# Performance work log

Measured on AMD Instinct MI355X. Metric: run time of the kernel, lower is better.

## Reference

```python
import jax, jax.numpy as jnp
import numpy as np

# static config matching init_kwargs
NODE, K, KER, STR = 32, 10, 5, 2
B, C = 8, 64
N = NODE * NODE          # 1024 nodes per sample
BN = B * N               # 8192 total nodes
OUT = (NODE - KER) // STR + 1
E = OUT * OUT            # local hyperedges per sample (196)
BN_EPS = 1e-5


def _local_block_diag():
    """Static block-diagonal local incidence matrix (BN, B*E), built once in numpy."""
    idx = np.arange(N).reshape(NODE, NODE)
    H_local = np.zeros((N, E), np.float32)
    e = 0
    for i in range(0, NODE - KER + 1, STR):
        for j in range(0, NODE - KER + 1, STR):
            H_local[idx[i:i + KER, j:j + KER].ravel(), e] = 1.0
            e += 1
    blk = np.zeros((BN, B * E), np.float32)
    for b in range(B):
        blk[b * N:(b + 1) * N, b * E:(b + 1) * E] = H_local
    return jnp.asarray(blk)


_LOCAL_BLK = _local_block_diag()


def setup_inputs() -> dict:
    key = jax.random.key(0)
    k1, k2 = jax.random.split(key, 2)
    x = jax.random.normal(k1, (B, N, C), jnp.float32)
    W_conv = jax.random.normal(k2, (C, C), jnp.float32) * 0.05
    b_conv = jnp.zeros((C,), jnp.float32)
    gamma = jnp.ones((C,), jnp.float32)
    beta = jnp.zeros((C,), jnp.float32)
    return {"x": x, "W_conv": W_conv, "b_conv": b_conv, "gamma": gamma, "beta": beta}


def reference(x, W_conv, b_conv, gamma, beta):
    xm = x.reshape(BN, C)                       # merged nodes (B*N, C)

    # --- hypergraph construction (no_grad in torch) ---
    xs = jax.lax.stop_gradient(xm)
    sq = jnp.sum(xs * xs, axis=-1, keepdims=True)
    dists = sq - 2.0 * (xs @ xs.T) + sq.T       # (BN, BN) pairwise sq-dists
    _, inds = jax.lax.top_k(-dists, K + 1)      # K+1 smallest distances
    # weights_function(prob=False) -> all ones; scatter incidence
    H = jnp.zeros((BN, BN), x.dtype).at[jnp.arange(BN)[:, None], inds].set(1.0)
    # Dv == K+1 for every row -> max_k = K+1 and the second topk gives new_H == H
    Hfull = jnp.concatenate([H, _LOCAL_BLK], axis=1)  # (BN, BN + B*E)

    # G = Dv^{-1/2} H W De^{-1} H^T Dv^{-1/2}, W = I, via diagonal scaling
    DV = Hfull.sum(axis=1)
    DE = jnp.maximum(Hfull.sum(axis=0), 1e-8)
    dv2 = DV ** -0.5
    A = dv2[:, None] * Hfull
    G = (A * (1.0 / DE)[None, :]) @ A.T          # (BN, BN)
    G = jax.lax.stop_gradient(G)

    # --- HGNN conv: linear -> G matmul -> BN (train stats) -> relu -> residual ---
    y = xm @ W_conv.T + b_conv                   # (BN, C)
    z = G @ y                                    # (BN, C)
    mu = z.mean(axis=0)
    var = z.var(axis=0)                          # biased, as torch BN training
    zn = (z - mu) / jnp.sqrt(var + BN_EPS) * gamma + beta
    out = jax.nn.relu(zn) + xm
    return out.reshape(B, N, C)
```

## Files before the change

### kernel.cpp

```cpp
#include <hip/hip_runtime.h>
#include <math.h>

#define BNTOT 8192
#define CH    64
#define KP1   11
#define NLOC  1568
#define CAP   1024
#define LCAP  64
#define MARGIN 2.5f

typedef __attribute__((ext_vector_type(8))) short short8;
typedef __attribute__((ext_vector_type(4))) float float4v;

__device__ __forceinline__ int pcnt(int p) {
  int lo = p - 4; if (lo < 0) lo = 0; lo += (lo & 1);
  int hi = p; if (hi > 26) hi = 26;
  return (hi >= lo) ? (((hi - lo) >> 1) + 1) : 0;
}
__device__ __forceinline__ float dv2_of(int u) {
  int node = u & 1023;
  int rr = node >> 5, cc = node & 31;
  int dv = KP1 + pcnt(rr) * pcnt(cc);
  return 1.0f / sqrtf((float)dv);
}
__device__ __forceinline__ unsigned short f2bf(float f) {
  unsigned u = __float_as_uint(f);
  unsigned r = (u + 0x7FFFu + ((u >> 16) & 1u)) >> 16;
  return (unsigned short)r;
}
__device__ __forceinline__ unsigned long long skey(float s, int idx) {
  unsigned u = __float_as_uint(s);
  u = (u & 0x80000000u) ? ~u : (u | 0x80000000u);
  return ((unsigned long long)u << 32) | (unsigned)idx;
}

__global__ void k_cast(const float* __restrict__ X, unsigned short* __restrict__ Xh,
                       float* __restrict__ sq) {
  int g = blockIdx.x * 256 + threadIdx.x;
  int lane = threadIdx.x & 63;
  float v = X[g];
  Xh[g] = f2bf(v);
  float s = v * v;
  #pragma unroll
  for (int off = 32; off >= 1; off >>= 1) s += __shfl_xor(s, off, 64);
  if (lane == 0) sq[g >> 6] = s;
}

__global__ __launch_bounds__(256)
void k_thrpart(const float* __restrict__ X, const float* __restrict__ sq,
               float* __restrict__ part) {
  const int tid = threadIdx.x, wave = tid >> 6, lane = tid & 63;
  const int rg = blockIdx.x >> 3, chunk = blockIdx.x & 7;
  const int row = rg * 64 + lane;
  float xr[CH];
  {
    const float4* xp = (const float4*)(X + (size_t)row * CH);
    #pragma unroll
    for (int k = 0; k < CH / 4; ++k) {
      float4 v = xp[k];
      xr[4*k+0] = v.x; xr[4*k+1] = v.y; xr[4*k+2] = v.z; xr[4*k+3] = v.w;
    }
  }
  float tv[KP1];
  #pragma unroll
  for (int t = 0; t < KP1; ++t) tv[t] = INFINITY;

  for (int s = 0; s < 32; ++s) {
    int j = __builtin_amdgcn_readfirstlane(((chunk * 4 + wave) * 32 + s) * 8);
    const float* cp = X + (size_t)j * CH;
    float d0 = 0.f, d1 = 0.f, d2 = 0.f, d3 = 0.f;
    #pragma unroll
    for (int k = 0; k < CH / 4; ++k) {
      d0 = fmaf(xr[4*k+0], cp[4*k+0], d0);
      d1 = fmaf(xr[4*k+1], cp[4*k+1], d1);
      d2 = fmaf(xr[4*k+2], cp[4*k+2], d2);
      d3 = fmaf(xr[4*k+3], cp[4*k+3], d3);
    }
    float cv = fmaf(-2.0f, (d0 + d1) + (d2 + d3), sq[j]);
    #pragma unroll
    for (int t = 0; t < KP1; ++t) {
      float lo = fminf(tv[t], cv), hi = fmaxf(tv[t], cv);
      tv[t] = lo; cv = hi;
    }
  }
  __shared__ float ls[4][64][KP1];
  #pragma unroll
  for (int t = 0; t < KP1; ++t) ls[wave][lane][t] = tv[t];
  __syncthreads();
  if (tid < 64) {
    float v[KP1];
    #pragma unroll
    for (int t = 0; t < KP1; ++t) v[t] = ls[0][tid][t];
    #pragma unroll
    for (int w = 1; w < 4; ++w)
      #pragma unroll
      for (int t = 0; t < KP1; ++t) {
        float cv = ls[w][tid][t];
        #pragma unroll
        for (int s2 = 0; s2 < KP1; ++s2) {
          float lo = fminf(v[s2], cv), hi = fmaxf(v[s2], cv);
          v[s2] = lo; cv = hi;
        }
      }
    size_t base = ((size_t)blockIdx.x * 64 + tid) * KP1;
    #pragma unroll
    for (int t = 0; t < KP1; ++t) part[base + t] = v[t];
  }
}

__global__ void k_thrmerge(const float* __restrict__ part, float* __restrict__ thr) {
  const int rg = blockIdx.x, lane = threadIdx.x;
  const int row = rg * 64 + lane;
  float v[KP1];
  {
    size_t b0 = ((size_t)(rg * 8) * 64 + lane) * KP1;
    #pragma unroll
    for (int t = 0; t < KP1; ++t) v[t] = part[b0 + t];
  }
  for (int c = 1; c < 8; ++c) {
    size_t b = ((size_t)(rg * 8 + c) * 64 + lane) * KP1;
    #pragma unroll
    for (int t = 0; t < KP1; ++t) {
      float cv = part[b + t];
      #pragma unroll
      for (int s2 = 0; s2 < KP1; ++s2) {
        float lo = fminf(v[s2], cv), hi = fmaxf(v[s2], cv);
        v[s2] = lo; cv = hi;
      }
    }
  }
  thr[row] = v[KP1 - 1] + MARGIN;
}

__global__ __launch_bounds__(256)
void k_filter(const unsigned short* __restrict__ Xh, const float* __restrict__ sq,
              const float* __restrict__ thr, int* __restrict__ cnt,
              unsigned short* __restrict__ cand) {
  __shared__ unsigned short lcand[64][LCAP + 2];
  __shared__ int lcnt[64];
  __shared__ int lbase[64];

  const int tid = threadIdx.x, wave = tid >> 6, lane = tid & 63;
  const int m = lane & 15, q = lane >> 4;
  const int rowbase = (blockIdx.x >> 5) * 64;
  const int colbase = (blockIdx.x & 31) * 256 + wave * 64;

  if (tid < 64) lcnt[tid] = 0;

  short8 a[4][2];
  #pragma unroll
  for (int rt = 0; rt < 4; ++rt)
    #pragma unroll
    for (int kc = 0; kc < 2; ++kc)
      a[rt][kc] = *(const short8*)(Xh + (size_t)(rowbase + rt * 16 + m) * CH + kc * 32 + q * 8);

  short8 b0[4], b1[4];
  float sqv[4];
  #pragma unroll
  for (int sub = 0; sub < 4; ++sub) {
    const int coln = colbase + sub * 16 + m;
    const short8* bp = (const short8*)(Xh + (size_t)coln * CH + q * 8);
    b0[sub] = bp[0];
    b1[sub] = bp[4];
    sqv[sub] = sq[coln];
  }

  float thrv[16];
  #pragma unroll
  for (int rt = 0; rt < 4; ++rt)
    #pragma unroll
    for (int r = 0; r < 4; ++r)
      thrv[rt * 4 + r] = thr[rowbase + rt * 16 + q * 4 + r];

  __syncthreads();

  const float4v cz = {0.f, 0.f, 0.f, 0.f};
  #pragma unroll
  for (int sub = 0; sub < 4; ++sub) {
    const int coln = colbase + sub * 16 + m;
    #pragma unroll
    for (int rt = 0; rt < 4; ++rt) {
      float4v c = __builtin_amdgcn_mfma_f32_16x16x32_bf16(a[rt][0], b0[sub], cz, 0, 0, 0);
      c = __builtin_amdgcn_mfma_f32_16x16x32_bf16(a[rt][1], b1[sub], c, 0, 0, 0);
      #pragma unroll
      for (int r = 0; r < 4; ++r) {
        float score = fmaf(-2.0f, c[r], sqv[sub]);
        if (score < thrv[rt * 4 + r]) {
          int rl = rt * 16 + q * 4 + r;
          int s = atomicAdd(&lcnt[rl], 1);
          if (s < LCAP) {
            lcand[rl][s] = (unsigned short)coln;
          } else {
            int gs = atomicAdd(&cnt[rowbase + rl], 1);
            if (gs < CAP) cand[(size_t)(rowbase + rl) * CAP + gs] = (unsigned short)coln;
          }
        }
      }
    }
  }

  __syncthreads();
  if (tid < 64) {
    int nl = lcnt[tid]; if (nl > LCAP) nl = LCAP;
    lbase[tid] = atomicAdd(&cnt[rowbase + tid], nl);
    lcnt[tid] = nl;
  }
  __syncthreads();
  if (tid < 64) {
    int nl = lcnt[tid], base = lbase[tid];
    unsigned short* dst = cand + (size_t)(rowbase + tid) * CAP;
    for (int s = 0; s < nl; ++s) {
      int g = base + s;
      if (g < CAP) dst[g] = lcand[tid][s];
    }
  }
}

__global__ __launch_bounds__(256)
void k_rescore(const float* __restrict__ X, const float* __restrict__ sq,
               const int* __restrict__ cnt, const unsigned short* __restrict__ cand,
               int* __restrict__ inds, int* __restrict__ DE) {
  const int tid = threadIdx.x, lane = tid & 63;
  const int row = __builtin_amdgcn_readfirstlane(blockIdx.x * 4 + (tid >> 6));

  float xr[CH];
  {
    const float4* xp = (const float4*)(X + (size_t)row * CH);
    #pragma unroll
    for (int k = 0; k < CH / 4; ++k) {
      float4 v = xp[k];
      xr[4*k+0] = v.x; xr[4*k+1] = v.y; xr[4*k+2] = v.z; xr[4*k+3] = v.w;
    }
  }
  int n = cnt[row]; if (n > CAP) n = CAP;

  float tv[KP1]; int ti[KP1];
  #pragma unroll
  for (int t = 0; t < KP1; ++t) { tv[t] = INFINITY; ti[t] = -1; }

  for (int s = lane; s < n; s += 64) {
    int cj = cand[(size_t)row * CAP + s];
    const float4* cp = (const float4*)(X + (size_t)cj * CH);
    float d0 = 0.f, d1 = 0.f, d2 = 0.f, d3 = 0.f;
    #pragma unroll
    for (int k = 0; k < CH / 4; ++k) {
      float4 v = cp[k];
      d0 = fmaf(xr[4*k+0], v.x, d0);
      d1 = fmaf(xr[4*k+1], v.y, d1);
      d2 = fmaf(xr[4*k+2], v.z, d2);
      d3 = fmaf(xr[4*k+3], v.w, d3);
    }
    float score = fmaf(-2.0f, (d0 + d1) + (d2 + d3), sq[cj]);
    if (score < tv[KP1 - 1]) {
      float cv = score; int ci = cj;
      #pragma unroll
      for (int t = 0; t < KP1; ++t) {
        bool sw = cv < tv[t];
        float nv = sw ? cv   : tv[t]; int ni = sw ? ci   : ti[t];
        float ov = sw ? tv[t] : cv;   int oi = sw ? ti[t] : ci;
        tv[t] = nv; ti[t] = ni; cv = ov; ci = oi;
      }
    }
  }

  unsigned long long cur = skey(tv[0], ti[0]);
  unsigned long long keep = 0;
  #pragma unroll
  for (int t = 0; t < KP1; ++t) {
    unsigned long long m = cur;
    #pragma unroll
    for (int off = 1; off < 64; off <<= 1) {
      unsigned lo = __shfl_xor((unsigned)m, off, 64);
      unsigned hi = __shfl_xor((unsigned)(m >> 32), off, 64);
      unsigned long long o = ((unsigned long long)hi << 32) | lo;
      m = (o < m) ? o : m;
    }
    if (lane == t) keep = m;
    if (cur == m) {
      #pragma unroll
      for (int q = 0; q < KP1 - 1; ++q) { tv[q] = tv[q+1]; ti[q] = ti[q+1]; }
      tv[KP1-1] = INFINITY; ti[KP1-1] = -1;
      cur = skey(tv[0], ti[0]);
    }
  }
  if (lane < KP1) {
    int idx = (int)(unsigned)(keep & 0xFFFFFFFFu);
    inds[(size_t)row * KP1 + lane] = idx;
    atomicAdd(&DE[idx], 1);
  }
}

__global__ void k_lin(const float* __restrict__ X, const float* __restrict__ W,
                      const float* __restrict__ bias, float* __restrict__ t) {
  int lane = threadIdx.x & 63;
  int wave = threadIdx.x >> 6;
  int rowbase = (blockIdx.x * 4 + wave) * 16;
  float wr[CH];
  {
    const float4* wp = (const float4*)(W + (size_t)lane * CH);
    #pragma unroll
    for (int k = 0; k < CH / 4; ++k) {
      float4 v = wp[k];
      wr[4*k+0] = v.x; wr[4*k+1] = v.y; wr[4*k+2] = v.z; wr[4*k+3] = v.w;
    }
  }
  float bc = bias[lane];
  for (int r = 0; r < 16; ++r) {
    int row = __builtin_amdgcn_readfirstlane(rowbase + r);
    const float* xp = X + (size_t)row * CH;
    float d0 = 0.f, d1 = 0.f, d2 = 0.f, d3 = 0.f;
    #pragma unroll
    for (int k = 0; k < CH / 4; ++k) {
      d0 = fmaf(wr[4*k+0], xp[4*k+0], d0);
      d1 = fmaf(wr[4*k+1], xp[4*k+1], d1);
      d2 = fmaf(wr[4*k+2], xp[4*k+2], d2);
      d3 = fmaf(wr[4*k+3], xp[4*k+3], d3);
    }
    float y = (d0 + d1) + (d2 + d3) + bc;
    t[(size_t)row * CH + lane] = y * dv2_of(row);
  }
}

__global__ void k_scatter(const float* __restrict__ t, const int* __restrict__ inds,
                          float* __restrict__ s_knn) {
  int c = threadIdx.x & 63;
  int u = blockIdx.x * 4 + (threadIdx.x >> 6);
  float val = t[(size_t)u * CH + c];
  int ub = __builtin_amdgcn_readfirstlane(u);
  const int* ip = inds + (size_t)ub * KP1;
  #pragma unroll
  for (int j = 0; j < KP1; ++j) {
    int e = ip[j];
    atomicAdd(&s_knn[(size_t)e * CH + c], val);
  }
}

__global__ void k_local(const float* __restrict__ t, float* __restrict__ s_loc) {
  int c = threadIdx.x & 63;
  int e = blockIdx.x * 4 + (threadIdx.x >> 6);
  int b  = e / 196;
  int le = e - b * 196;
  int pi = le / 14;
  int pj = le - pi * 14;
  int base = b * 1024 + (pi * 2) * 32 + pj * 2;
  float acc = 0.f;
  #pragma unroll
  for (int di = 0; di < 5; ++di)
    #pragma unroll
    for (int dj = 0; dj < 5; ++dj)
      acc += t[(size_t)(base + di * 32 + dj) * CH + c];
  s_loc[(size_t)e * CH + c] = acc * (1.0f / 25.0f);
}

__global__ void k_gather(const float* __restrict__ s_knn, const float* __restrict__ s_loc,
                         const int* __restrict__ inds, const int* __restrict__ DE,
                         float* __restrict__ z) {
  int c = threadIdx.x & 63;
  int u = blockIdx.x * 4 + (threadIdx.x >> 6);
  int ub = __builtin_amdgcn_readfirstlane(u);
  const int* ip = inds + (size_t)ub * KP1;
  float acc = 0.f;
  #pragma unroll
  for (int j = 0; j < KP1; ++j) {
    int e = ip[j];
    float invde = 1.0f / (float)DE[e];
    acc += s_knn[(size_t)e * CH + c] * invde;
  }
  int node = ub & 1023, b = ub >> 10;
  int rr = node >> 5, cc = node & 31;
  int i0 = rr - 4; if (i0 < 0) i0 = 0; i0 += (i0 & 1);
  int i1 = rr; if (i1 > 26) i1 = 26;
  int j0 = cc - 4; if (j0 < 0) j0 = 0; j0 += (j0 & 1);
  int j1 = cc; if (j1 > 26) j1 = 26;
  for (int i = i0; i <= i1; i += 2)
    for (int jj = j0; jj <= j1; jj += 2) {
      int e = b * 196 + (i >> 1) * 14 + (jj >> 1);
      acc += s_loc[(size_t)e * CH + c];
    }
  z[(size_t)ub * CH + c] = acc * dv2_of(ub);
}

__global__ void k_bnpart(const float* __restrict__ z, float* __restrict__ part,
                         float* __restrict__ partsq) {
  int c = threadIdx.x & 63;
  int rq = threadIdx.x >> 6;
  int blk = blockIdx.x;
  float s = 0.f, s2 = 0.f;
  for (int k = 0; k < 16; ++k) {
    float v = z[(size_t)(blk * 64 + rq * 16 + k) * CH + c];
    s += v; s2 += v * v;
  }
  __shared__ float ls[4][CH], ls2[4][CH];
  ls[rq][c] = s; ls2[rq][c] = s2;
  __syncthreads();
  if (rq == 0) {
    part[(size_t)blk * CH + c]   = ls[0][c] + ls[1][c] + ls[2][c] + ls[3][c];
    partsq[(size_t)blk * CH + c] = ls2[0][c] + ls2[1][c] + ls2[2][c] + ls2[3][c];
  }
}

__global__ void k_bnfin(const float* __restrict__ part, const float* __restrict__ partsq,
                        float* __restrict__ mu, float* __restrict__ rstd) {
  int c = threadIdx.x;
  float s = 0.f, s2 = 0.f;
  for (int b = 0; b < 128; ++b) { s += part[(size_t)b * CH + c]; s2 += partsq[(size_t)b * CH + c]; }
  float m = s * (1.0f / (float)BNTOT);
  float var = s2 * (1.0f / (float)BNTOT) - m * m;
  mu[c] = m;
  rstd[c] = 1.0f / sqrtf(var + 1e-5f);
}

__global__ void k_out(const float* __restrict__ z, const float* __restrict__ X,
                      const float* __restrict__ mu, const float* __restrict__ rstd,
                      const float* __restrict__ gamma, const float* __restrict__ beta,
                      float* __restrict__ out) {
  int c = threadIdx.x & 63;
  int u = blockIdx.x * 4 + (threadIdx.x >> 6);
  size_t idx = (size_t)u * CH + c;
  float zn = (z[idx] - mu[c]) * rstd[c] * gamma[c] + beta[c];
  out[idx] = fmaxf(zn, 0.f) + X[idx];
}

extern "C" void kernel_launch(void* const* d_in, const int* in_sizes, int n_in,
                              void* d_out, int out_size, void* d_ws, size_t ws_size,
                              hipStream_t stream) {
  const float* X     = (const float*)d_in[0];
  const float* W     = (const float*)d_in[1];
  const float* bias  = (const float*)d_in[2];
  const float* gamma = (const float*)d_in[3];
  const float* beta  = (const float*)d_in[4];
  float* out = (float*)d_out;

  float* ws = (float*)d_ws;
  float* sq      = ws;
  float* thr     = sq + 8192;
  float* t       = thr + 8192;
  float* s_loc   = t + 524288;
  float* z       = s_loc + 100352;
  float* part    = z + 524288;
  float* partsq  = part + 8192;
  float* mu      = partsq + 8192;
  float* rstd    = mu + 64;
  float* thrpart = rstd + 64;
  int*   inds    = (int*)(thrpart + 720896);
  unsigned short* Xh   = (unsigned short*)(inds + 90112);
  unsigned short* cand = Xh + 524288;
  int*   cnt    = (int*)(cand + (size_t)8192 * CAP);
  int*   DE     = cnt + 8192;
  float* s_knn  = (float*)(DE + 8192);

  hipMemsetAsync(cnt, 0, (size_t)(8192 + 8192 + 524288) * 4, stream);

  k_cast    <<<2048, 256, 0, stream>>>(X, Xh, sq);
  k_thrpart <<<1024, 256, 0, stream>>>(X, sq, thrpart);
  k_thrmerge<<<128, 64, 0, stream>>>(thrpart, thr);
  k_filter  <<<4096, 256, 0, stream>>>(Xh, sq, thr, cnt, cand);
  k_rescore <<<2048, 256, 0, stream>>>(X, sq, cnt, cand, inds, DE);
  k_lin     <<<128, 256, 0, stream>>>(X, W, bias, t);
  k_scatter <<<BNTOT / 4, 256, 0, stream>>>(t, inds, s_knn);
  k_local   <<<NLOC / 4, 256, 0, stream>>>(t, s_loc);
  k_gather  <<<BNTOT / 4, 256, 0, stream>>>(s_knn, s_loc, inds, DE, z);
  k_bnpart  <<<128, 256, 0, stream>>>(z, part, partsq);
  k_bnfin   <<<1, 64, 0, stream>>>(part, partsq, mu, rstd);
  k_out     <<<BNTOT / 4, 256, 0, stream>>>(z, X, mu, rstd, gamma, beta, out);

  (void)in_sizes; (void)n_in; (void)out_size; (void)ws_size;
}
```

Measured before the change: 258.8 us.

## Store bf16 filter scores with candidates and prune exact rescoring by cutoff

The filter kernel now stores each candidate's approximate bf16 score alongside its column index, and tightens the margin and candidate capacities. The rescore kernel finds the 11th-best approximate score with a wave reduction and recomputes exact fp32 distances only for candidates within DELTA of it. If a row overflows the smaller capacity, it falls back to a brute-force scan over all nodes. The linear kernel also gets more blocks, each handling fewer rows, and its row loop is unrolled. The risks are missing true neighbours if the bf16 error exceeds the margins, and a slow fallback on overflowing rows.

```diff
diff --git a/kernel.cpp b/kernel.cpp
--- a/kernel.cpp
+++ b/kernel.cpp
@@ -5,9 +5,10 @@
 #define CH    64
 #define KP1   11
 #define NLOC  1568
-#define CAP   1024
-#define LCAP  64
-#define MARGIN 2.5f
+#define CAP   256
+#define LCAP  32
+#define MARGIN 1.0f
+#define DELTA  2.0f
 
 typedef __attribute__((ext_vector_type(8))) short short8;
 typedef __attribute__((ext_vector_type(4))) float float4v;
@@ -135,8 +136,8 @@
 __global__ __launch_bounds__(256)
 void k_filter(const unsigned short* __restrict__ Xh, const float* __restrict__ sq,
               const float* __restrict__ thr, int* __restrict__ cnt,
-              unsigned short* __restrict__ cand) {
-  __shared__ unsigned short lcand[64][LCAP + 2];
+              uint2* __restrict__ cand) {
+  __shared__ uint2 lcand[64][LCAP];
   __shared__ int lcnt[64];
   __shared__ int lbase[64];
 
@@ -187,12 +188,13 @@
         float score = fmaf(-2.0f, c[r], sqv[sub]);
         if (score < thrv[rt * 4 + r]) {
           int rl = rt * 16 + q * 4 + r;
+          uint2 ent; ent.x = (unsigned)coln; ent.y = __float_as_uint(score);
           int s = atomicAdd(&lcnt[rl], 1);
           if (s < LCAP) {
-            lcand[rl][s] = (unsigned short)coln;
+            lcand[rl][s] = ent;
           } else {
             int gs = atomicAdd(&cnt[rowbase + rl], 1);
-            if (gs < CAP) cand[(size_t)(rowbase + rl) * CAP + gs] = (unsigned short)coln;
+            if (gs < CAP) cand[(size_t)(rowbase + rl) * CAP + gs] = ent;
           }
         }
       }
@@ -208,7 +210,7 @@
   __syncthreads();
   if (tid < 64) {
     int nl = lcnt[tid], base = lbase[tid];
-    unsigned short* dst = cand + (size_t)(rowbase + tid) * CAP;
+    uint2* dst = cand + (size_t)(rowbase + tid) * CAP;
     for (int s = 0; s < nl; ++s) {
       int g = base + s;
       if (g < CAP) dst[g] = lcand[tid][s];
@@ -218,7 +220,7 @@
 
 __global__ __launch_bounds__(256)
 void k_rescore(const float* __restrict__ X, const float* __restrict__ sq,
-               const int* __restrict__ cnt, const unsigned short* __restrict__ cand,
+               const int* __restrict__ cnt, const uint2* __restrict__ cand,
                int* __restrict__ inds, int* __restrict__ DE) {
   const int tid = threadIdx.x, lane = tid & 63;
   const int row = __builtin_amdgcn_readfirstlane(blockIdx.x * 4 + (tid >> 6));
@@ -232,33 +234,88 @@
       xr[4*k+0] = v.x; xr[4*k+1] = v.y; xr[4*k+2] = v.z; xr[4*k+3] = v.w;
     }
   }
-  int n = cnt[row]; if (n > CAP) n = CAP;
+  const int nraw = cnt[row];
 
   float tv[KP1]; int ti[KP1];
   #pragma unroll
   for (int t = 0; t < KP1; ++t) { tv[t] = INFINITY; ti[t] = -1; }
 
-  for (int s = lane; s < n; s += 64) {
-    int cj = cand[(size_t)row * CAP + s];
-    const float4* cp = (const float4*)(X + (size_t)cj * CH);
-    float d0 = 0.f, d1 = 0.f, d2 = 0.f, d3 = 0.f;
-    #pragma unroll
-    for (int k = 0; k < CH / 4; ++k) {
-      float4 v = cp[k];
-      d0 = fmaf(xr[4*k+0], v.x, d0);
-      d1 = fmaf(xr[4*k+1], v.y, d1);
-      d2 = fmaf(xr[4*k+2], v.z, d2);
-      d3 = fmaf(xr[4*k+3], v.w, d3);
-    }
-    float score = fmaf(-2.0f, (d0 + d1) + (d2 + d3), sq[cj]);
-    if (score < tv[KP1 - 1]) {
-      float cv = score; int ci = cj;
+  if (nraw <= CAP) {
+    const int n = nraw;
+    const int slotcnt = (n + 63) >> 6;
+
+    float bsc[4]; int bcol[4];
+    #pragma unroll
+    for (int a = 0; a < 4; ++a) { bsc[a] = INFINITY; bcol[a] = -1; }
+    for (int a = 0; a < slotcnt; ++a) {
+      int s = a * 64 + lane;
+      if (s < n) {
+        uint2 e = cand[(size_t)row * CAP + s];
+        bcol[a] = (int)e.x; bsc[a] = __uint_as_float(e.y);
+      }
+    }
+    float curf = bsc[0];
+    #pragma unroll
+    for (int a = 1; a < 4; ++a) curf = fminf(curf, bsc[a]);
+    float c11 = INFINITY;
+    #pragma unroll
+    for (int t = 0; t < KP1; ++t) {
+      float mw = curf;
       #pragma unroll
-      for (int t = 0; t < KP1; ++t) {
-        bool sw = cv < tv[t];
-        float nv = sw ? cv   : tv[t]; int ni = sw ? ci   : ti[t];
-        float ov = sw ? tv[t] : cv;   int oi = sw ? ti[t] : ci;
-        tv[t] = nv; ti[t] = ni; cv = ov; ci = oi;
+      for (int off = 1; off < 64; off <<= 1) mw = fminf(mw, __shfl_xor(mw, off, 64));
+      if (t == KP1 - 1) c11 = mw;
+      if (curf == mw) curf = INFINITY;
+    }
+    const float cutoff = c11 + DELTA;
+
+    for (int a = 0; a < slotcnt; ++a) {
+      if (bsc[a] <= cutoff) {
+        int cj = bcol[a];
+        const float4* cp = (const float4*)(X + (size_t)cj * CH);
+        float d0 = 0.f, d1 = 0.f, d2 = 0.f, d3 = 0.f;
+        #pragma unroll
+        for (int k = 0; k < CH / 4; ++k) {
+          float4 v = cp[k];
+          d0 = fmaf(xr[4*k+0], v.x, d0);
+          d1 = fmaf(xr[4*k+1], v.y, d1);
+          d2 = fmaf(xr[4*k+2], v.z, d2);
+          d3 = fmaf(xr[4*k+3], v.w, d3);
+        }
+        float score = fmaf(-2.0f, (d0 + d1) + (d2 + d3), sq[cj]);
+        if (score < tv[KP1 - 1]) {
+          float cv = score; int ci = cj;
+          #pragma unroll
+          for (int t = 0; t < KP1; ++t) {
+            bool sw = cv < tv[t];
+            float nv = sw ? cv   : tv[t]; int ni = sw ? ci   : ti[t];
+            float ov = sw ? tv[t] : cv;   int oi = sw ? ti[t] : ci;
+            tv[t] = nv; ti[t] = ni; cv = ov; ci = oi;
+          }
+        }
+      }
+    }
+  } else {
+    for (int s = lane; s < BNTOT; s += 64) {
+      const float4* cp = (const float4*)(X + (size_t)s * CH);
+      float d0 = 0.f, d1 = 0.f, d2 = 0.f, d3 = 0.f;
+      #pragma unroll
+      for (int k = 0; k < CH / 4; ++k) {
+        float4 v = cp[k];
+        d0 = fmaf(xr[4*k+0], v.x, d0);
+        d1 = fmaf(xr[4*k+1], v.y, d1);
+        d2 = fmaf(xr[4*k+2], v.z, d2);
+        d3 = fmaf(xr[4*k+3], v.w, d3);
+      }
+      float score = fmaf(-2.0f, (d0 + d1) + (d2 + d3), sq[s]);
+      if (score < tv[KP1 - 1]) {
+        float cv = score; int ci = s;
+        #pragma unroll
+        for (int t = 0; t < KP1; ++t) {
+          bool sw = cv < tv[t];
+          float nv = sw ? cv   : tv[t]; int ni = sw ? ci   : ti[t];
+          float ov = sw ? tv[t] : cv;   int oi = sw ? ti[t] : ci;
+          tv[t] = nv; ti[t] = ni; cv = ov; ci = oi;
+        }
       }
     }
   }
@@ -267,16 +324,16 @@
   unsigned long long keep = 0;
   #pragma unroll
   for (int t = 0; t < KP1; ++t) {
-    unsigned long long m = cur;
+    unsigned long long mw = cur;
     #pragma unroll
     for (int off = 1; off < 64; off <<= 1) {
-      unsigned lo = __shfl_xor((unsigned)m, off, 64);
-      unsigned hi = __shfl_xor((unsigned)(m >> 32), off, 64);
+      unsigned lo = __shfl_xor((unsigned)mw, off, 64);
+      unsigned hi = __shfl_xor((unsigned)(mw >> 32), off, 64);
       unsigned long long o = ((unsigned long long)hi << 32) | lo;
-      m = (o < m) ? o : m;
-    }
-    if (lane == t) keep = m;
-    if (cur == m) {
+      mw = (o < mw) ? o : mw;
+    }
+    if (lane == t) keep = mw;
+    if (cur == mw) {
       #pragma unroll
       for (int q = 0; q < KP1 - 1; ++q) { tv[q] = tv[q+1]; ti[q] = ti[q+1]; }
       tv[KP1-1] = INFINITY; ti[KP1-1] = -1;
@@ -284,7 +341,7 @@
     }
   }
   if (lane < KP1) {
-    int idx = (int)(unsigned)(keep & 0xFFFFFFFFu);
+    int idx = (int)(unsigned)(keep & 0xFFFFFFFFull);
     inds[(size_t)row * KP1 + lane] = idx;
     atomicAdd(&DE[idx], 1);
   }
@@ -294,7 +351,7 @@
                       const float* __restrict__ bias, float* __restrict__ t) {
   int lane = threadIdx.x & 63;
   int wave = threadIdx.x >> 6;
-  int rowbase = (blockIdx.x * 4 + wave) * 16;
+  int rowbase = (blockIdx.x * 4 + wave) * 4;
   float wr[CH];
   {
     const float4* wp = (const float4*)(W + (size_t)lane * CH);
@@ -305,7 +362,8 @@
     }
   }
   float bc = bias[lane];
-  for (int r = 0; r < 16; ++r) {
+  #pragma unroll
+  for (int r = 0; r < 4; ++r) {
     int row = __builtin_amdgcn_readfirstlane(rowbase + r);
     const float* xp = X + (size_t)row * CH;
     float d0 = 0.f, d1 = 0.f, d2 = 0.f, d3 = 0.f;
@@ -443,8 +501,8 @@
   float* rstd    = mu + 64;
   float* thrpart = rstd + 64;
   int*   inds    = (int*)(thrpart + 720896);
-  unsigned short* Xh   = (unsigned short*)(inds + 90112);
-  unsigned short* cand = Xh + 524288;
+  unsigned short* Xh = (unsigned short*)(inds + 90112);
+  uint2* cand    = (uint2*)(Xh + 524288);
   int*   cnt    = (int*)(cand + (size_t)8192 * CAP);
   int*   DE     = cnt + 8192;
   float* s_knn  = (float*)(DE + 8192);
@@ -456,7 +514,7 @@
   k_thrmerge<<<128, 64, 0, stream>>>(thrpart, thr);
   k_filter  <<<4096, 256, 0, stream>>>(Xh, sq, thr, cnt, cand);
   k_rescore <<<2048, 256, 0, stream>>>(X, sq, cnt, cand, inds, DE);
-  k_lin     <<<128, 256, 0, stream>>>(X, W, bias, t);
+  k_lin     <<<512, 256, 0, stream>>>(X, W, bias, t);
   k_scatter <<<BNTOT / 4, 256, 0, stream>>>(t, inds, s_knn);
   k_local   <<<NLOC / 4, 256, 0, stream>>>(t, s_loc);
   k_gather  <<<BNTOT / 4, 256, 0, stream>>>(s_knn, s_loc, inds, DE, z);
```

Result: faster. 237.3 us (-8.3%).
